# Performance work log

Hardware: AMD Instinct MI355X
Metric: run time of the kernel (lower is better)

## Reference

```python
import jax, jax.numpy as jnp
import numpy as np

N = 50000       # nodes
E = 1600000     # edges (before self loops)
IN = 128        # in_dim
H = 4           # heads
C = 64          # hidden_channels per head
F = H * C       # 256 concat width
OUT = 10
BN_EPS = 1e-5
NEG_SLOPE = 0.2  # PyG GATConv default


def _gat_conv(x, eidx, W, a_src, a_dst, b):
    # x: [N, F_in]; eidx: [2, E2] with self loops (row0=src, row1=dst)
    xw = (x @ W).reshape(N, H, C)                      # [N, H, C]
    s = jnp.einsum('nhc,hc->nh', xw, a_src)            # [N, H]
    d = jnp.einsum('nhc,hc->nh', xw, a_dst)            # [N, H]
    src, dst = eidx[0], eidx[1]
    alpha = jax.nn.leaky_relu(s[src] + d[dst], NEG_SLOPE)   # [E2, H]
    # scatter-softmax over incoming edges of each dst node (numerically stable)
    m = jax.ops.segment_max(alpha, dst, num_segments=N)
    m = jax.lax.stop_gradient(jnp.where(jnp.isfinite(m), m, 0.0))
    ex = jnp.exp(alpha - m[dst])                       # [E2, H]
    denom = jax.ops.segment_sum(ex, dst, num_segments=N)
    w = ex / (denom[dst] + 1e-16)                      # [E2, H]
    # weighted scatter-add aggregation
    out = jax.ops.segment_sum(w[:, :, None] * xw[src], dst, num_segments=N)  # [N,H,C]
    return out.reshape(N, F) + b


def _batchnorm(h, gamma, beta):
    # training-mode batch stats over the node axis
    mu = jnp.mean(h, axis=0)
    var = jnp.var(h, axis=0)
    return (h - mu) * jax.lax.rsqrt(var + BN_EPS) * gamma + beta


def setup_inputs() -> dict:
    key = jax.random.key(0)
    ks = jax.random.split(key, 12)
    sc = 0.05
    x = jax.random.normal(ks[0], (N, IN), jnp.float32)
    edge_index = jax.random.randint(ks[1], (2, E), 0, N, jnp.int64)
    return {
        'x': x,
        'edge_index': edge_index,
        'W1': jax.random.normal(ks[2], (IN, F), jnp.float32) * sc,
        'a_src1': jax.random.normal(ks[3], (H, C), jnp.float32) * sc,
        'a_dst1': jax.random.normal(ks[4], (H, C), jnp.float32) * sc,
        'b1': jnp.zeros((F,), jnp.float32),
        'W2': jax.random.normal(ks[5], (F, F), jnp.float32) * sc,
        'a_src2': jax.random.normal(ks[6], (H, C), jnp.float32) * sc,
        'a_dst2': jax.random.normal(ks[7], (H, C), jnp.float32) * sc,
        'b2': jnp.zeros((F,), jnp.float32),
        'g1': jnp.ones((F,), jnp.float32),
        'be1': jnp.zeros((F,), jnp.float32),
        'g2': jnp.ones((F,), jnp.float32),
        'be2': jnp.zeros((F,), jnp.float32),
        'Wc': jax.random.normal(ks[8], (F, OUT), jnp.float32) * sc,
        'bc': jnp.zeros((OUT,), jnp.float32),
    }


def reference(x, edge_index, W1, a_src1, a_dst1, b1, W2, a_src2, a_dst2, b2,
              g1, be1, g2, be2, Wc, bc):
    # add self loops (PyG GATConv default add_self_loops=True)
    loops = jnp.arange(N, dtype=edge_index.dtype)
    eidx = jnp.concatenate([edge_index, jnp.stack([loops, loops])], axis=1)
    h = jax.nn.relu(_gat_conv(x, eidx, W1, a_src1, a_dst1, b1))
    h = _batchnorm(h, g1, be1)          # dropout(0.2) treated as identity (eval)
    h = jax.nn.relu(_gat_conv(h, eidx, W2, a_src2, a_dst2, b2))
    h = _batchnorm(h, g2, be2)
    out = h @ Wc + bc                   # [N, OUT]
    return out[None]                    # [1, N, OUT]; squeeze(-1) is a no-op for OUT>1
```

## Files before the change

kernel.cpp:

```cpp
#include <hip/hip_runtime.h>

#define N_NODES 50000
#define E_EDGES 1600000
#define E2 (E_EDGES + N_NODES)
#define HEADS 4
#define F 256
#define OUTC 10
#define BN_EPS 1e-5f
#define NEG_SLOPE 0.2f
#define NSLICE 64
#define SB 1024
#define NB ((N_NODES + SB - 1) / SB)

#define CXB (N_NODES * 128 / 4 / 256)
#define CWB 128
#define CDB ((E2 + 255) / 256)

static_assert(N_NODES % 4 == 0, "grid_nw exact");

typedef __attribute__((ext_vector_type(8))) short short8;
typedef __attribute__((ext_vector_type(4))) float f32x4;

__device__ __forceinline__ unsigned short f2bf(float f) {
    unsigned int u = __float_as_uint(f);
    unsigned int r = (u + 0x7fffu + ((u >> 16) & 1u)) >> 16;
    return (unsigned short)r;
}
__device__ __forceinline__ float bf2f(unsigned short b) {
    return __uint_as_float(((unsigned int)b) << 16);
}

__global__ __launch_bounds__(256) void mega_prep(
    const float* __restrict__ X, unsigned short* __restrict__ Xb,
    const float* __restrict__ W1, unsigned short* __restrict__ WT,
    const int* __restrict__ eidx, int* __restrict__ deg)
{
    const int b = blockIdx.x;
    const int t = threadIdx.x;
    if (b < CXB) {
        const int i = b * 256 + t;
        float4 v = reinterpret_cast<const float4*>(X)[i];
        ushort4 o = { f2bf(v.x), f2bf(v.y), f2bf(v.z), f2bf(v.w) };
        reinterpret_cast<ushort4*>(Xb)[i] = o;
    } else if (b < CXB + CWB) {
        const int k = b - CXB;
        WT[t * 128 + k] = f2bf(W1[k * 256 + t]);
    } else {
        const int e = (b - CXB - CWB) * 256 + t;
        if (e < E2) {
            int dst = (e < E_EDGES) ? eidx[E_EDGES + e] : e - E_EDGES;
            atomicAdd(&deg[dst], 1);
        }
    }
}

__global__ __launch_bounds__(SB) void scan_blocks(
    const int* __restrict__ deg, int* __restrict__ rowptr, int* __restrict__ bsum)
{
    __shared__ int sm[SB];
    const int t = threadIdx.x;
    const int idx = blockIdx.x * SB + t;
    int v = (idx < N_NODES) ? deg[idx] : 0;
    sm[t] = v;
    __syncthreads();
    for (int off = 1; off < SB; off <<= 1) {
        int u = (t >= off) ? sm[t - off] : 0;
        __syncthreads();
        sm[t] += u;
        __syncthreads();
    }
    if (idx < N_NODES) rowptr[idx] = sm[t] - v;
    if (t == SB - 1) bsum[blockIdx.x] = sm[t];
}

__global__ __launch_bounds__(SB) void scan_add2(
    int* __restrict__ rowptr, const int* __restrict__ bsum)
{
    __shared__ int boff_s;
    if (threadIdx.x == 0) {
        int run = 0;
        for (int b = 0; b < (int)blockIdx.x; b++) run += bsum[b];
        boff_s = run;
        if (blockIdx.x == 0) {
            int tot = 0;
            for (int b = 0; b < NB; b++) tot += bsum[b];
            rowptr[N_NODES] = tot;
        }
    }
    __syncthreads();
    const int idx = blockIdx.x * SB + threadIdx.x;
    if (idx < N_NODES) rowptr[idx] += boff_s;
}

__global__ __launch_bounds__(256) void scatter_edges(
    const int* __restrict__ eidx, const int* __restrict__ rowptr,
    int* __restrict__ cursor, int* __restrict__ esrc)
{
    int e = blockIdx.x * blockDim.x + threadIdx.x;
    if (e >= E2) return;
    int src, dst;
    if (e < E_EDGES) { src = eidx[e]; dst = eidx[E_EDGES + e]; }
    else             { src = dst = e - E_EDGES; }
    int pos = atomicAdd(&cursor[dst], 1);
    esrc[rowptr[dst] + pos] = src;
}

template<int K, bool BROW>
__global__ __launch_bounds__(256) void gemm_sd(
    const unsigned short* __restrict__ A, const unsigned short* __restrict__ BT,
    const float* __restrict__ brow, const float* __restrict__ a_src,
    const float* __restrict__ a_dst, unsigned short* __restrict__ C,
    float* __restrict__ S, float* __restrict__ D)
{
    const int t = threadIdx.x;
    const int wave = t >> 6, lane = t & 63;
    const int lo = lane & 15, hi = lane >> 4;
    const int row0 = blockIdx.x * 64;
    const int nbase = wave * 64;

    int arow[4];
#pragma unroll
    for (int m = 0; m < 4; m++)
        arow[m] = min(row0 + m * 16 + lo, N_NODES - 1);

    f32x4 acc[4][4];
#pragma unroll
    for (int m = 0; m < 4; m++)
#pragma unroll
        for (int n = 0; n < 4; n++)
            acc[m][n] = (f32x4){0.f, 0.f, 0.f, 0.f};

    for (int k0 = 0; k0 < K; k0 += 32) {
        const int kk = k0 + hi * 8;
        short8 af[4], bfr[4];
#pragma unroll
        for (int m = 0; m < 4; m++)
            af[m] = *reinterpret_cast<const short8*>(A + (size_t)arow[m] * K + kk);
#pragma unroll
        for (int n = 0; n < 4; n++)
            bfr[n] = *reinterpret_cast<const short8*>(BT + (size_t)(nbase + n * 16 + lo) * K + kk);
#pragma unroll
        for (int m = 0; m < 4; m++)
#pragma unroll
            for (int n = 0; n < 4; n++)
                acc[m][n] = __builtin_amdgcn_mfma_f32_16x16x32_bf16(
                    af[m], bfr[n], acc[m][n], 0, 0, 0);
    }

    float bb[4], asv[4], adv[4];
#pragma unroll
    for (int n = 0; n < 4; n++) {
        int col = nbase + n * 16 + lo;
        bb[n]  = BROW ? brow[col] : 0.f;
        asv[n] = a_src[col];
        adv[n] = a_dst[col];
    }

#pragma unroll
    for (int m = 0; m < 4; m++) {
#pragma unroll
        for (int i = 0; i < 4; i++) {
            const int row = row0 + m * 16 + hi * 4 + i;
            const bool ok = row < N_NODES;
            float ps = 0.f, pd = 0.f;
#pragma unroll
            for (int n = 0; n < 4; n++) {
                float v = acc[m][n][i] + bb[n];
                ps += v * asv[n];
                pd += v * adv[n];
                if (ok) C[(size_t)row * F + nbase + n * 16 + lo] = f2bf(v);
            }
#pragma unroll
            for (int off = 1; off < 16; off <<= 1) {
                ps += __shfl_xor(ps, off, 64);
                pd += __shfl_xor(pd, off, 64);
            }
            if (lo == 0 && ok) {
                S[row * HEADS + wave] = ps;
                D[row * HEADS + wave] = pd;
            }
        }
    }
}

__global__ __launch_bounds__(256) void gat_aggregate(
    const int* __restrict__ rowptr, const int* __restrict__ esrc,
    const float* __restrict__ S, const float* __restrict__ D,
    const unsigned short* __restrict__ XWb, const float* __restrict__ bias,
    unsigned short* __restrict__ Hb, float* __restrict__ stp)
{
    __shared__ int   sbuf[4][64];
    __shared__ float wbuf[4][64][4];
    __shared__ float red_s[4][F];
    __shared__ float red_q[4][F];
    const int wv   = threadIdx.x >> 6;
    const int lane = threadIdx.x & 63;
    const int dst  = blockIdx.x * 4 + wv;
    const int beg = rowptr[dst], end = rowptr[dst + 1];
    const int h = lane >> 4;
    const float4 d4 = *reinterpret_cast<const float4*>(D + dst * HEADS);

    float ax = 0.f, ay = 0.f, az = 0.f, aw = 0.f, den = 0.f;

    for (int i = beg; i < end; i += 64) {
        const int nb = min(64, end - i);
        const bool valid = (i + lane < end);
        const int mysrc = valid ? esrc[i + lane] : 0;
        float4 w4 = {0.f, 0.f, 0.f, 0.f};
        if (valid) {
            const float4 s4 = *reinterpret_cast<const float4*>(S + mysrc * HEADS);
            float z;
            z = s4.x + d4.x; w4.x = __expf(z > 0.f ? z : NEG_SLOPE * z);
            z = s4.y + d4.y; w4.y = __expf(z > 0.f ? z : NEG_SLOPE * z);
            z = s4.z + d4.z; w4.z = __expf(z > 0.f ? z : NEG_SLOPE * z);
            z = s4.w + d4.w; w4.w = __expf(z > 0.f ? z : NEG_SLOPE * z);
        }
        sbuf[wv][lane] = mysrc;
        *reinterpret_cast<float4*>(&wbuf[wv][lane][0]) = w4;

        int j = 0;
        for (; j + 7 < nb; j += 8) {
            int s0 = sbuf[wv][j + 0], s1 = sbuf[wv][j + 1];
            int s2 = sbuf[wv][j + 2], s3 = sbuf[wv][j + 3];
            int s4i = sbuf[wv][j + 4], s5 = sbuf[wv][j + 5];
            int s6 = sbuf[wv][j + 6], s7 = sbuf[wv][j + 7];
            float w0 = wbuf[wv][j + 0][h], w1 = wbuf[wv][j + 1][h];
            float w2 = wbuf[wv][j + 2][h], w3 = wbuf[wv][j + 3][h];
            float w4f = wbuf[wv][j + 4][h], w5 = wbuf[wv][j + 5][h];
            float w6 = wbuf[wv][j + 6][h], w7 = wbuf[wv][j + 7][h];
            ushort4 x0 = *reinterpret_cast<const ushort4*>(XWb + (size_t)s0 * F + lane * 4);
            ushort4 x1 = *reinterpret_cast<const ushort4*>(XWb + (size_t)s1 * F + lane * 4);
            ushort4 x2 = *reinterpret_cast<const ushort4*>(XWb + (size_t)s2 * F + lane * 4);
            ushort4 x3 = *reinterpret_cast<const ushort4*>(XWb + (size_t)s3 * F + lane * 4);
            ushort4 x4 = *reinterpret_cast<const ushort4*>(XWb + (size_t)s4i * F + lane * 4);
            ushort4 x5 = *reinterpret_cast<const ushort4*>(XWb + (size_t)s5 * F + lane * 4);
            ushort4 x6 = *reinterpret_cast<const ushort4*>(XWb + (size_t)s6 * F + lane * 4);
            ushort4 x7 = *reinterpret_cast<const ushort4*>(XWb + (size_t)s7 * F + lane * 4);
            ax += w0 * bf2f(x0.x) + w1 * bf2f(x1.x) + w2 * bf2f(x2.x) + w3 * bf2f(x3.x)
                + w4f * bf2f(x4.x) + w5 * bf2f(x5.x) + w6 * bf2f(x6.x) + w7 * bf2f(x7.x);
            ay += w0 * bf2f(x0.y) + w1 * bf2f(x1.y) + w2 * bf2f(x2.y) + w3 * bf2f(x3.y)
                + w4f * bf2f(x4.y) + w5 * bf2f(x5.y) + w6 * bf2f(x6.y) + w7 * bf2f(x7.y);
            az += w0 * bf2f(x0.z) + w1 * bf2f(x1.z) + w2 * bf2f(x2.z) + w3 * bf2f(x3.z)
                + w4f * bf2f(x4.z) + w5 * bf2f(x5.z) + w6 * bf2f(x6.z) + w7 * bf2f(x7.z);
            aw += w0 * bf2f(x0.w) + w1 * bf2f(x1.w) + w2 * bf2f(x2.w) + w3 * bf2f(x3.w)
                + w4f * bf2f(x4.w) + w5 * bf2f(x5.w) + w6 * bf2f(x6.w) + w7 * bf2f(x7.w);
            den += ((w0 + w1) + (w2 + w3)) + ((w4f + w5) + (w6 + w7));
        }
        for (; j < nb; j++) {
            int   src = sbuf[wv][j];
            float w = wbuf[wv][j][h];
            ushort4 xv = *reinterpret_cast<const ushort4*>(XWb + (size_t)src * F + lane * 4);
            ax += w * bf2f(xv.x); ay += w * bf2f(xv.y);
            az += w * bf2f(xv.z); aw += w * bf2f(xv.w);
            den += w;
        }
    }

    const float inv = 1.f / (den + 1e-16f);
    float4 bv = *reinterpret_cast<const float4*>(bias + lane * 4);
    float v0 = ax * inv + bv.x, v1 = ay * inv + bv.y;
    float v2 = az * inv + bv.z, v3 = aw * inv + bv.w;
    v0 = v0 > 0.f ? v0 : 0.f; v1 = v1 > 0.f ? v1 : 0.f;
    v2 = v2 > 0.f ? v2 : 0.f; v3 = v3 > 0.f ? v3 : 0.f;
    ushort4 o = { f2bf(v0), f2bf(v1), f2bf(v2), f2bf(v3) };
    *reinterpret_cast<ushort4*>(Hb + (size_t)dst * F + lane * 4) = o;

    f32x4 rs = {v0, v1, v2, v3};
    f32x4 rq = {v0 * v0, v1 * v1, v2 * v2, v3 * v3};
    *reinterpret_cast<f32x4*>(&red_s[wv][lane * 4]) = rs;
    *reinterpret_cast<f32x4*>(&red_q[wv][lane * 4]) = rq;
    __syncthreads();
    const int ch = threadIdx.x;
    float s = (red_s[0][ch] + red_s[1][ch]) + (red_s[2][ch] + red_s[3][ch]);
    float q = (red_q[0][ch] + red_q[1][ch]) + (red_q[2][ch] + red_q[3][ch]);
    float* slice = stp + (size_t)(blockIdx.x & (NSLICE - 1)) * (2 * F);
    atomicAdd(&slice[ch], s);
    atomicAdd(&slice[F + ch], q);
}

__global__ __launch_bounds__(256) void fold1(
    const float* __restrict__ stp, const float* __restrict__ g,
    const float* __restrict__ be, const float* __restrict__ W2,
    unsigned short* __restrict__ WT2b, float* __restrict__ brow)
{
    __shared__ float sc_l[F], sh_l[F];
    const int t = threadIdx.x;
    float s = 0.f, q = 0.f;
    for (int b = 0; b < NSLICE; b++) {
        s += stp[(size_t)b * 2 * F + t];
        q += stp[(size_t)b * 2 * F + F + t];
    }
    const float inv_n = 1.f / (float)N_NODES;
    float mu = s * inv_n;
    float var = q * inv_n - mu * mu;
    float sc = rsqrtf(var + BN_EPS) * g[t];
    sc_l[t] = sc;
    sh_l[t] = be[t] - mu * sc;
    __syncthreads();
    if (blockIdx.x < 32) {
        const int k0 = blockIdx.x * 8;
#pragma unroll
        for (int kk = 0; kk < 8; kk++)
            WT2b[(size_t)t * F + k0 + kk] = f2bf(W2[(size_t)(k0 + kk) * F + t] * sc_l[k0 + kk]);
    } else {
        float acc = 0.f;
        for (int k = 0; k < F; k++)
            acc += sh_l[k] * W2[(size_t)k * F + t];
        brow[t] = acc;
    }
}

__global__ __launch_bounds__(256) void fold_wc(
    const float* __restrict__ stp, const float* __restrict__ g,
    const float* __restrict__ be, const float* __restrict__ Wc,
    const float* __restrict__ bc, float* __restrict__ Wcp, float* __restrict__ bcp)
{
    __shared__ float sc_l[F], sh_l[F];
    __shared__ float red[256][OUTC];
    const int t = threadIdx.x;
    float s = 0.f, q = 0.f;
    for (int b = 0; b < NSLICE; b++) {
        s += stp[(size_t)b * 2 * F + t];
        q += stp[(size_t)b * 2 * F + F + t];
    }
    const float inv_n = 1.f / (float)N_NODES;
    float mu = s * inv_n;
    float var = q * inv_n - mu * mu;
    float sc = rsqrtf(var + BN_EPS) * g[t];
    sc_l[t] = sc;
    sh_l[t] = be[t] - mu * sc;
    const float sh_t = be[t] - mu * sc;
#pragma unroll
    for (int o = 0; o < OUTC; o++) {
        float wv = Wc[t * OUTC + o];
        Wcp[t * OUTC + o] = wv * sc;
        red[t][o] = sh_t * wv;
    }
    __syncthreads();
    for (int off = 128; off > 0; off >>= 1) {
        if (t < off) {
#pragma unroll
            for (int o = 0; o < OUTC; o++)
                red[t][o] += red[t + off][o];
        }
        __syncthreads();
    }
    if (t < OUTC) bcp[t] = bc[t] + red[0][t];
}

__global__ __launch_bounds__(256) void classifier(
    const unsigned short* __restrict__ Hb, const float* __restrict__ Wcp,
    const float* __restrict__ bcp, float* __restrict__ out)
{
    __shared__ float wls[F][OUTC + 1];
    const int t = threadIdx.x;
    for (int i = t; i < F * OUTC; i += 256)
        wls[i / OUTC][i % OUTC] = Wcp[i];
    __syncthreads();

    const int wave = t >> 6, lane = t & 63;
    const int n = blockIdx.x * 4 + wave;
    if (n >= N_NODES) return;

    float v[4];
#pragma unroll
    for (int j = 0; j < 4; j++)
        v[j] = bf2f(Hb[(size_t)n * F + j * 64 + lane]);

    float acc[OUTC];
#pragma unroll
    for (int o = 0; o < OUTC; o++) acc[o] = 0.f;
#pragma unroll
    for (int j = 0; j < 4; j++)
#pragma unroll
        for (int o = 0; o < OUTC; o++)
            acc[o] += v[j] * wls[j * 64 + lane][o];

#pragma unroll
    for (int off = 32; off > 0; off >>= 1)
#pragma unroll
        for (int o = 0; o < OUTC; o++)
            acc[o] += __shfl_xor(acc[o], off, 64);

    if (lane == 0) {
#pragma unroll
        for (int o = 0; o < OUTC; o++)
            out[(size_t)n * OUTC + o] = acc[o] + bcp[o];
    }
}

extern "C" void kernel_launch(void* const* d_in, const int* in_sizes, int n_in,
                              void* d_out, int out_size, void* d_ws, size_t ws_size,
                              hipStream_t stream)
{
    const float* x   = (const float*)d_in[0];
    const int*   ei  = (const int*)d_in[1];
    const float* W1  = (const float*)d_in[2];
    const float* as1 = (const float*)d_in[3];
    const float* ad1 = (const float*)d_in[4];
    const float* b1  = (const float*)d_in[5];
    const float* W2  = (const float*)d_in[6];
    const float* as2 = (const float*)d_in[7];
    const float* ad2 = (const float*)d_in[8];
    const float* b2  = (const float*)d_in[9];
    const float* g1  = (const float*)d_in[10];
    const float* be1 = (const float*)d_in[11];
    const float* g2  = (const float*)d_in[12];
    const float* be2 = (const float*)d_in[13];
    const float* Wc  = (const float*)d_in[14];
    const float* bc  = (const float*)d_in[15];
    float* out = (float*)d_out;

    char* w = (char*)d_ws;
    int*   deg   = (int*)w;                      w += (size_t)N_NODES * 4;
    int*   cursor= (int*)w;                      w += (size_t)N_NODES * 4;
    float* stp1  = (float*)w;                    w += (size_t)NSLICE * 2 * F * 4;
    float* stp2  = (float*)w;                    w += (size_t)NSLICE * 2 * F * 4;
    const size_t zero_bytes = (size_t)N_NODES * 8 + (size_t)NSLICE * 2 * F * 8;

    unsigned short* Xb   = (unsigned short*)w;   w += (size_t)N_NODES * 128 * 2;
    unsigned short* XWb  = (unsigned short*)w;   w += (size_t)N_NODES * F * 2;
    unsigned short* Hb   = (unsigned short*)w;   w += (size_t)N_NODES * F * 2;
    unsigned short* WT1b = (unsigned short*)w;   w += 256 * 128 * 2;
    unsigned short* WT2b = (unsigned short*)w;   w += 256 * 256 * 2;
    float* Wcp   = (float*)w;                    w += F * OUTC * 4;
    float* bcp   = (float*)w;                    w += 64;
    float* brow2 = (float*)w;                    w += F * 4;
    float* Sv    = (float*)w;                    w += (size_t)N_NODES * HEADS * 4;
    float* Dv    = (float*)w;                    w += (size_t)N_NODES * HEADS * 4;
    int* rowp    = (int*)w;                      w += (size_t)(N_NODES + 1) * 4;
    int* bsum    = (int*)w;                      w += NB * 4;
    int* esrc    = (int*)w;

    const int grid_e    = (E2 + 255) / 256;
    const int grid_nw   = N_NODES / 4;
    const int grid_gemm = (N_NODES + 63) / 64;
    const int grid_prep = CXB + CWB + CDB;

    hipMemsetAsync(deg, 0, zero_bytes, stream);
    mega_prep<<<grid_prep, 256, 0, stream>>>(x, Xb, W1, WT1b, ei, deg);
    scan_blocks<<<NB, SB, 0, stream>>>(deg, rowp, bsum);
    scan_add2<<<NB, SB, 0, stream>>>(rowp, bsum);
    scatter_edges<<<grid_e, 256, 0, stream>>>(ei, rowp, cursor, esrc);

    gemm_sd<128, false><<<grid_gemm, 256, 0, stream>>>(
        Xb, WT1b, nullptr, as1, ad1, XWb, Sv, Dv);
    gat_aggregate<<<grid_nw, 256, 0, stream>>>(rowp, esrc, Sv, Dv, XWb, b1, Hb, stp1);
    fold1<<<33, 256, 0, stream>>>(stp1, g1, be1, W2, WT2b, brow2);

    gemm_sd<256, true><<<grid_gemm, 256, 0, stream>>>(
        Hb, WT2b, brow2, as2, ad2, XWb, Sv, Dv);
    gat_aggregate<<<grid_nw, 256, 0, stream>>>(rowp, esrc, Sv, Dv, XWb, b2, Hb, stp2);
    fold_wc<<<1, 256, 0, stream>>>(stp2, g2, be2, Wc, bc, Wcp, bcp);

    classifier<<<grid_nw, 256, 0, stream>>>(Hb, Wcp, bcp, out);
}
```

Measured before the change: 562.6 us.

## Partition degree count and edge scatter by destination range per XCD

The degree-count and CSR scatter kernels now launch 8 blocks per 2048-edge chunk, and each block handles only the edges whose destination falls in one eighth of the node range. Consecutive block IDs map to different XCDs, so each XCD's atomics and writes should stay within its own slice of deg/cursor/esrc and hit its local L2 rather than bouncing across dies. The cost is that every edge's destination index is read eight times, and each block keeps only about one eighth of its threads busy.

```diff
diff --git a/kernel.cpp b/kernel.cpp
--- a/kernel.cpp
+++ b/kernel.cpp
@@ -12,11 +12,17 @@
 #define SB 1024
 #define NB ((N_NODES + SB - 1) / SB)
 
+#define NXCD 8
+#define NR (N_NODES / NXCD)
+#define EPB 2048
+#define NCHUNK ((E2 + EPB - 1) / EPB)
+
 #define CXB (N_NODES * 128 / 4 / 256)
 #define CWB 128
-#define CDB ((E2 + 255) / 256)
-
-static_assert(N_NODES % 4 == 0, "grid_nw exact");
+#define CDB (NXCD * NCHUNK)
+
+static_assert(N_NODES % (4) == 0, "grid_nw exact");
+static_assert(N_NODES % NXCD == 0, "ranges exact");
 
 typedef __attribute__((ext_vector_type(8))) short short8;
 typedef __attribute__((ext_vector_type(4))) float f32x4;
@@ -46,9 +52,16 @@
         const int k = b - CXB;
         WT[t * 128 + k] = f2bf(W1[k * 256 + t]);
     } else {
-        const int e = (b - CXB - CWB) * 256 + t;
-        if (e < E2) {
+        const int b2 = b - CXB - CWB;
+        const int r = b2 & (NXCD - 1);
+        const int chunk = b2 >> 3;
+        const int lo = r * NR;
+        const int base = chunk * EPB;
+        for (int i = t; i < EPB; i += 256) {
+            const int e = base + i;
+            if (e >= E2) break;
             int dst = (e < E_EDGES) ? eidx[E_EDGES + e] : e - E_EDGES;
+            if ((unsigned)(dst - lo) >= (unsigned)NR) continue;
             atomicAdd(&deg[dst], 1);
         }
     }
@@ -92,17 +105,23 @@
     if (idx < N_NODES) rowptr[idx] += boff_s;
 }
 
-__global__ __launch_bounds__(256) void scatter_edges(
+__global__ __launch_bounds__(256) void scatter_edges8(
     const int* __restrict__ eidx, const int* __restrict__ rowptr,
     int* __restrict__ cursor, int* __restrict__ esrc)
 {
-    int e = blockIdx.x * blockDim.x + threadIdx.x;
-    if (e >= E2) return;
-    int src, dst;
-    if (e < E_EDGES) { src = eidx[e]; dst = eidx[E_EDGES + e]; }
-    else             { src = dst = e - E_EDGES; }
-    int pos = atomicAdd(&cursor[dst], 1);
-    esrc[rowptr[dst] + pos] = src;
+    const int r = blockIdx.x & (NXCD - 1);
+    const int chunk = blockIdx.x >> 3;
+    const int lo = r * NR;
+    const int base = chunk * EPB;
+    for (int i = threadIdx.x; i < EPB; i += 256) {
+        const int e = base + i;
+        if (e >= E2) break;
+        int dst = (e < E_EDGES) ? eidx[E_EDGES + e] : e - E_EDGES;
+        if ((unsigned)(dst - lo) >= (unsigned)NR) continue;
+        int src = (e < E_EDGES) ? eidx[e] : dst;
+        int pos = atomicAdd(&cursor[dst], 1);
+        esrc[rowptr[dst] + pos] = src;
+    }
 }
 
 template<int K, bool BROW>
@@ -432,16 +451,16 @@
     int* bsum    = (int*)w;                      w += NB * 4;
     int* esrc    = (int*)w;
 
-    const int grid_e    = (E2 + 255) / 256;
     const int grid_nw   = N_NODES / 4;
     const int grid_gemm = (N_NODES + 63) / 64;
     const int grid_prep = CXB + CWB + CDB;
+    const int grid_sc   = NXCD * NCHUNK;
 
     hipMemsetAsync(deg, 0, zero_bytes, stream);
     mega_prep<<<grid_prep, 256, 0, stream>>>(x, Xb, W1, WT1b, ei, deg);
     scan_blocks<<<NB, SB, 0, stream>>>(deg, rowp, bsum);
     scan_add2<<<NB, SB, 0, stream>>>(rowp, bsum);
-    scatter_edges<<<grid_e, 256, 0, stream>>>(ei, rowp, cursor, esrc);
+    scatter_edges8<<<grid_sc, 256, 0, stream>>>(ei, rowp, cursor, esrc);
 
     gemm_sd<128, false><<<grid_gemm, 256, 0, stream>>>(
         Xb, WT1b, nullptr, as1, ad1, XWb, Sv, Dv);
```

Measured after the change: 532.9 us. -5.3%, faster.
